# Kernel optimization log

Hardware: AMD Instinct MI355X
Metric: run time of the kernel (lower is better)

Reference implementation:

```python
import jax, jax.numpy as jnp
import numpy as np

N_NODES = 50000
N_EDGES = 300000
D = 256
N_RELS = 500


def setup_inputs() -> dict:
    key = jax.random.key(0)
    ks = jax.random.split(key, 12)
    s = 1.0 / np.sqrt(D)  # keep activations O(1) through the dense transforms
    return {
        "h": jax.random.normal(ks[0], (N_NODES, D), dtype=jnp.float32),
        "prev_h": jax.random.normal(ks[1], (N_NODES, D), dtype=jnp.float32),
        "emb_rel": jax.random.normal(ks[2], (N_RELS, D), dtype=jnp.float32),
        "norm": jax.random.uniform(ks[3], (N_NODES, 1), dtype=jnp.float32),
        "weight_neighbor": jax.random.normal(ks[4], (D, D), dtype=jnp.float32) * s,
        "loop_weight": jax.random.normal(ks[5], (D, D), dtype=jnp.float32) * s,
        "evolve_loop_weight": jax.random.normal(ks[6], (D, D), dtype=jnp.float32) * s,
        "skip_connect_weight": jax.random.normal(ks[7], (D, D), dtype=jnp.float32) * s,
        "skip_connect_bias": jnp.zeros((D,), dtype=jnp.float32),
        "src": jax.random.randint(ks[8], (N_EDGES,), 0, N_NODES),
        "dst": jax.random.randint(ks[9], (N_EDGES,), 0, N_NODES),
        "etype": jax.random.randint(ks[10], (N_EDGES,), 0, N_RELS),
    }


def reference(h, prev_h, emb_rel, norm, weight_neighbor, loop_weight,
              evolve_loop_weight, skip_connect_weight, skip_connect_bias,
              src, dst, etype):
    n_nodes = h.shape[0]
    # msg_func: per-edge gather of src features + relation embedding, dense transform
    msg = (h[src] + emb_rel[etype]) @ weight_neighbor          # [E, D]
    # fn.sum: segment-sum messages into destination nodes
    agg = jax.ops.segment_sum(msg, dst, num_segments=n_nodes)  # [N, D]
    # apply_func: multiply by per-node norm
    agg = agg * norm
    # self-loop: loop_weight where in_degree > 0, evolve_loop_weight otherwise
    in_deg = jax.ops.segment_sum(jnp.ones_like(dst), dst, num_segments=n_nodes)
    has_in = (in_deg > 0)[:, None]
    loop_message = jnp.where(has_in, h @ loop_weight, h @ evolve_loop_weight)
    # skip connection gate
    skip_weight = jax.nn.sigmoid(prev_h @ skip_connect_weight + skip_connect_bias)
    node_repr = skip_weight * (agg + loop_message) + (1.0 - skip_weight) * prev_h
    return jax.nn.relu(node_repr)
```

## Files before the change

### kernel.cpp

```cpp
#include <hip/hip_runtime.h>
#include <hip/hip_bf16.h>
#include <cstdint>
#include <cstddef>

#define N_NODES 50000
#define N_EDGES 300000
#define DIM     256
#define KTOT    768

#define SCAN_BLK  256
#define SCAN_NBLK ((N_NODES + SCAN_BLK - 1) / SCAN_BLK)

typedef unsigned short u16;
typedef __attribute__((ext_vector_type(8))) short short8v;
typedef __attribute__((ext_vector_type(4))) float float4v;

static __device__ __forceinline__ u16 f2bf(float f) {
    union { float f; unsigned u; } v; v.f = f;
    unsigned u = v.u;
    unsigned r = u + 0x7FFFu + ((u >> 16) & 1u);
    return (u16)(r >> 16);
}

__global__ void conv_kernel(const float* __restrict__ h, const float* __restrict__ ph,
                            u16* __restrict__ Xh, u16* __restrict__ Xp) {
    int i = blockIdx.x * blockDim.x + threadIdx.x;
    int e0 = i * 8;
    if (e0 >= 2 * N_NODES * DIM) return;
    const float* src; u16* dst; int off;
    if (e0 < N_NODES * DIM) { src = h;  dst = Xh; off = e0; }
    else                    { src = ph; dst = Xp; off = e0 - N_NODES * DIM; }
    float4 a = *(const float4*)(src + off);
    float4 b = *(const float4*)(src + off + 4);
    u16 o[8] = { f2bf(a.x), f2bf(a.y), f2bf(a.z), f2bf(a.w),
                 f2bf(b.x), f2bf(b.y), f2bf(b.z), f2bf(b.w) };
    *(uint4*)(dst + off) = *(const uint4*)o;
}

__global__ void wt_kernel(const float* __restrict__ Wn, const float* __restrict__ Wl,
                          const float* __restrict__ Wsc, u16* __restrict__ Wt) {
    int k = blockIdx.x;
    int d = threadIdx.x;
    const float* W = (k < 256) ? Wn : ((k < 512) ? Wl : Wsc);
    int kk = k & 255;
    Wt[(size_t)d * KTOT + k] = f2bf(W[kk * DIM + d]);
}

__global__ void hist_kernel(const int* __restrict__ dstv, int* __restrict__ deg) {
    int e = blockIdx.x * 256 + threadIdx.x;
    if (e < N_EDGES) atomicAdd(&deg[dstv[e]], 1);
}

__global__ void scanA_kernel(const int* __restrict__ deg, int* __restrict__ excl_local,
                             int* __restrict__ block_sum) {
    __shared__ int sdata[SCAN_BLK];
    int t = threadIdx.x, i = blockIdx.x * SCAN_BLK + t;
    int v = (i < N_NODES) ? deg[i] : 0;
    sdata[t] = v;
    __syncthreads();
    for (int off = 1; off < SCAN_BLK; off <<= 1) {
        int u = (t >= off) ? sdata[t - off] : 0;
        __syncthreads();
        sdata[t] += u;
        __syncthreads();
    }
    if (i < N_NODES) excl_local[i] = sdata[t] - v;
    if (t == SCAN_BLK - 1) block_sum[blockIdx.x] = sdata[t];
}

__global__ void scanB_kernel(const int* __restrict__ block_sum, int* __restrict__ block_base,
                             int* __restrict__ offsets) {
    __shared__ int sdata[SCAN_NBLK];
    int t = threadIdx.x;
    int v = (t < SCAN_NBLK) ? block_sum[t] : 0;
    if (t < SCAN_NBLK) sdata[t] = v;
    __syncthreads();
    for (int off = 1; off < SCAN_NBLK; off <<= 1) {
        int u = (t >= off && t < SCAN_NBLK) ? sdata[t - off] : 0;
        __syncthreads();
        if (t < SCAN_NBLK) sdata[t] += u;
        __syncthreads();
    }
    if (t < SCAN_NBLK) block_base[t] = sdata[t] - v;
    if (t == SCAN_NBLK - 1) offsets[N_NODES] = sdata[t];
}

__global__ void scanC_kernel(const int* __restrict__ excl_local, const int* __restrict__ block_base,
                             int* __restrict__ offsets, int* __restrict__ cursor) {
    int i = blockIdx.x * SCAN_BLK + threadIdx.x;
    if (i < N_NODES) {
        int e = block_base[blockIdx.x] + excl_local[i];
        offsets[i] = e; cursor[i] = e;
    }
}

__global__ void scatter_kernel(const int* __restrict__ src, const int* __restrict__ dstv,
                               const int* __restrict__ et, int* __restrict__ cursor,
                               int* __restrict__ es, int* __restrict__ ee) {
    int e = blockIdx.x * 256 + threadIdx.x;
    if (e >= N_EDGES) return;
    int d = dstv[e];
    int pos = atomicAdd(&cursor[d], 1);
    es[pos] = src[e];
    ee[pos] = et[e];
}

__global__ void agg_kernel(const float* __restrict__ h, const float* __restrict__ emb,
                           const float* __restrict__ norm, const int* __restrict__ offsets,
                           const int* __restrict__ es, const int* __restrict__ ee,
                           u16* __restrict__ Xa, int* __restrict__ wl_count, int* __restrict__ wl) {
    int wave = (blockIdx.x * 256 + threadIdx.x) >> 6;
    int lane = threadIdx.x & 63;
    if (wave >= N_NODES) return;
    int n = wave;
    int s0 = offsets[n], s1 = offsets[n + 1];
    int c4 = lane * 4;
    float4 acc = make_float4(0.f, 0.f, 0.f, 0.f);
    for (int e = s0; e < s1; e++) {
        int s = es[e], t = ee[e];
        float4 hv = *(const float4*)(h   + (size_t)s * DIM + c4);
        float4 ev = *(const float4*)(emb + (size_t)t * DIM + c4);
        acc.x += hv.x + ev.x; acc.y += hv.y + ev.y;
        acc.z += hv.z + ev.z; acc.w += hv.w + ev.w;
    }
    float nr = norm[n];
    u16 o[4] = { f2bf(acc.x * nr), f2bf(acc.y * nr), f2bf(acc.z * nr), f2bf(acc.w * nr) };
    *(ushort4*)(Xa + (size_t)n * DIM + c4) = *(const ushort4*)o;
    if (lane == 0 && s1 == s0) { int idx = atomicAdd(wl_count, 1); wl[idx] = n; }
}

#define LDSP 72
__launch_bounds__(256, 2)
__global__ void gemm_kernel(const u16* __restrict__ Xa, const u16* __restrict__ Xh,
                            const u16* __restrict__ Xp, const u16* __restrict__ Wt,
                            const float* __restrict__ prev_h, const float* __restrict__ bias,
                            float* __restrict__ out) {
    __shared__ u16 Xs[64 * LDSP];
    __shared__ u16 Ws[256 * LDSP];
    int tid = threadIdx.x;
    int wave = tid >> 6, lane = tid & 63, q = lane >> 4, m16 = lane & 15;
    int m0 = blockIdx.x * 64;

    float4v acc1[4][4], acc2[4][4];
#pragma unroll
    for (int i = 0; i < 4; i++)
#pragma unroll
        for (int j = 0; j < 4; j++) { acc1[i][j] = (float4v)0.f; acc2[i][j] = (float4v)0.f; }

    int xr = tid >> 3, xc = (tid & 7) * 8;
    int wp = tid & 7, wd = tid >> 3;
    int xrow0 = min(m0 + xr, N_NODES - 1);
    int xrow1 = min(m0 + xr + 32, N_NODES - 1);

    for (int kt = 0; kt < 12; kt++) {
        const u16* Xsrc = (kt < 4) ? Xa : ((kt < 8) ? Xh : Xp);
        int koff = (kt & 3) * 64;
        *(uint4*)(&Xs[xr * LDSP + xc]) =
            *(const uint4*)(Xsrc + (size_t)xrow0 * DIM + koff + xc);
        *(uint4*)(&Xs[(xr + 32) * LDSP + xc]) =
            *(const uint4*)(Xsrc + (size_t)xrow1 * DIM + koff + xc);
#pragma unroll
        for (int it = 0; it < 8; it++) {
            int d = wd + it * 32;
            *(uint4*)(&Ws[d * LDSP + wp * 8]) =
                *(const uint4*)(Wt + (size_t)d * KTOT + kt * 64 + wp * 8);
        }
        __syncthreads();
#pragma unroll
        for (int kk = 0; kk < 2; kk++) {
            short8v af[4], bfr[4];
#pragma unroll
            for (int mi = 0; mi < 4; mi++)
                af[mi] = *(const short8v*)(&Xs[(mi * 16 + m16) * LDSP + kk * 32 + q * 8]);
#pragma unroll
            for (int ni = 0; ni < 4; ni++)
                bfr[ni] = *(const short8v*)(&Ws[(wave * 64 + ni * 16 + m16) * LDSP + kk * 32 + q * 8]);
            if (kt < 8) {
#pragma unroll
                for (int mi = 0; mi < 4; mi++)
#pragma unroll
                    for (int ni = 0; ni < 4; ni++)
                        acc1[mi][ni] = __builtin_amdgcn_mfma_f32_16x16x32_bf16(
                            af[mi], bfr[ni], acc1[mi][ni], 0, 0, 0);
            } else {
#pragma unroll
                for (int mi = 0; mi < 4; mi++)
#pragma unroll
                    for (int ni = 0; ni < 4; ni++)
                        acc2[mi][ni] = __builtin_amdgcn_mfma_f32_16x16x32_bf16(
                            af[mi], bfr[ni], acc2[mi][ni], 0, 0, 0);
            }
        }
        __syncthreads();
    }

#pragma unroll
    for (int mi = 0; mi < 4; mi++) {
#pragma unroll
        for (int ni = 0; ni < 4; ni++) {
            int d = wave * 64 + ni * 16 + m16;
            float b = bias[d];
#pragma unroll
            for (int r = 0; r < 4; r++) {
                int node = m0 + mi * 16 + q * 4 + r;
                if (node < N_NODES) {
                    float S  = acc2[mi][ni][r] + b;
                    float sw = 1.f / (1.f + __expf(-S));
                    float ph = prev_h[(size_t)node * DIM + d];
                    float v  = sw * acc1[mi][ni][r] + (1.f - sw) * ph;
                    out[(size_t)node * DIM + d] = fmaxf(v, 0.f);
                }
            }
        }
    }
}

__global__ void fixup_kernel(const float* __restrict__ h, const float* __restrict__ prev_h,
                             const float* __restrict__ We, const float* __restrict__ Wsc,
                             const float* __restrict__ bias, const int* __restrict__ wl_count,
                             const int* __restrict__ wl, float* __restrict__ out) {
    __shared__ float ph[DIM], hh[DIM];
    int d = threadIdx.x;
    int cnt = *wl_count;
    for (int i = blockIdx.x; i < cnt; i += gridDim.x) {
        int n = wl[i];
        ph[d] = prev_h[(size_t)n * DIM + d];
        hh[d] = h[(size_t)n * DIM + d];
        __syncthreads();
        float s = 0.f, l = 0.f;
        for (int k = 0; k < DIM; k++) {
            s += ph[k] * Wsc[k * DIM + d];
            l += hh[k] * We[k * DIM + d];
        }
        float sw = 1.f / (1.f + __expf(-(s + bias[d])));
        float v = sw * l + (1.f - sw) * ph[d];
        out[(size_t)n * DIM + d] = fmaxf(v, 0.f);
        __syncthreads();
    }
}

extern "C" void kernel_launch(void* const* d_in, const int* in_sizes, int n_in,
                              void* d_out, int out_size, void* d_ws, size_t ws_size,
                              hipStream_t stream) {
    const float* h      = (const float*)d_in[0];
    const float* prev_h = (const float*)d_in[1];
    const float* emb    = (const float*)d_in[2];
    const float* norm   = (const float*)d_in[3];
    const float* Wn     = (const float*)d_in[4];
    const float* Wl     = (const float*)d_in[5];
    const float* We     = (const float*)d_in[6];
    const float* Wsc    = (const float*)d_in[7];
    const float* bias   = (const float*)d_in[8];
    const int*   src    = (const int*)d_in[9];
    const int*   dstv   = (const int*)d_in[10];
    const int*   et     = (const int*)d_in[11];
    float* out = (float*)d_out;

    char* ws = (char*)d_ws;
    size_t off = 0;
    auto alloc = [&](size_t bytes) -> char* {
        char* p = ws + off; off += (bytes + 255) & ~(size_t)255; return p;
    };
    u16* Xa      = (u16*)alloc((size_t)N_NODES * DIM * 2);
    u16* Xh      = (u16*)alloc((size_t)N_NODES * DIM * 2);
    u16* Xp      = (u16*)alloc((size_t)N_NODES * DIM * 2);
    u16* Wt      = (u16*)alloc((size_t)DIM * KTOT * 2);
    int* deg     = (int*)alloc((size_t)N_NODES * 4);
    int* wlcnt   = (int*)alloc(16);
    int* wl      = (int*)alloc((size_t)N_NODES * 4);
    int* offsets = (int*)alloc((size_t)(N_NODES + 1) * 4);
    int* cursor  = (int*)alloc((size_t)N_NODES * 4);
    int* es      = (int*)alloc((size_t)N_EDGES * 4);
    int* ee      = (int*)alloc((size_t)N_EDGES * 4);
    int* excl    = (int*)alloc((size_t)N_NODES * 4);
    int* bsum    = (int*)alloc((size_t)SCAN_NBLK * 4);
    int* bbase   = (int*)alloc((size_t)SCAN_NBLK * 4);

    hipMemsetAsync(deg, 0, (size_t)N_NODES * 4, stream);
    hipMemsetAsync(wlcnt, 0, 4, stream);

    conv_kernel<<<(2 * N_NODES * DIM / 8 + 255) / 256, 256, 0, stream>>>(h, prev_h, Xh, Xp);
    wt_kernel<<<KTOT, 256, 0, stream>>>(Wn, Wl, Wsc, Wt);
    hist_kernel<<<(N_EDGES + 255) / 256, 256, 0, stream>>>(dstv, deg);
    scanA_kernel<<<SCAN_NBLK, SCAN_BLK, 0, stream>>>(deg, excl, bsum);
    scanB_kernel<<<1, SCAN_BLK, 0, stream>>>(bsum, bbase, offsets);
    scanC_kernel<<<SCAN_NBLK, SCAN_BLK, 0, stream>>>(excl, bbase, offsets, cursor);
    scatter_kernel<<<(N_EDGES + 255) / 256, 256, 0, stream>>>(src, dstv, et, cursor, es, ee);
    agg_kernel<<<(N_NODES + 3) / 4, 256, 0, stream>>>(h, emb, norm, offsets, es, ee, Xa, wlcnt, wl);
    gemm_kernel<<<(N_NODES + 63) / 64, 256, 0, stream>>>(Xa, Xh, Xp, Wt, prev_h, bias, out);
    fixup_kernel<<<256, 256, 0, stream>>>(h, prev_h, We, Wsc, bias, wlcnt, wl, out);
}
```

Measured before the change: 353.2 us.

## Fuse fp32-to-bf16 conversion into GEMM, pack edge indices, enlarge GEMM tile

Removes the separate conversion kernel by converting h and prev_h rows to bf16 while loading them into shared memory inside the GEMM, which avoids writing and rereading two bf16 copies of the node features. Source index and relation type are packed into one 32-bit word per edge, cutting index traffic in scatter and aggregation at the cost of an integer divide per edge. The GEMM tile grows to 128 rows with 512 threads, so each weight tile is reused across more rows. The fp32 loads into the GEMM are wider than the bf16 loads they replace, and the larger tile leaves fewer blocks.

Measured after the change: 367.9 us. 4.2% more time.

```diff
diff --git a/kernel.cpp b/kernel.cpp
--- a/kernel.cpp
+++ b/kernel.cpp
@@ -7,6 +7,7 @@
 #define N_EDGES 300000
 #define DIM     256
 #define KTOT    768
+#define N_RELS  500
 
 #define SCAN_BLK  256
 #define SCAN_NBLK ((N_NODES + SCAN_BLK - 1) / SCAN_BLK)
@@ -20,21 +21,6 @@
     unsigned u = v.u;
     unsigned r = u + 0x7FFFu + ((u >> 16) & 1u);
     return (u16)(r >> 16);
-}
-
-__global__ void conv_kernel(const float* __restrict__ h, const float* __restrict__ ph,
-                            u16* __restrict__ Xh, u16* __restrict__ Xp) {
-    int i = blockIdx.x * blockDim.x + threadIdx.x;
-    int e0 = i * 8;
-    if (e0 >= 2 * N_NODES * DIM) return;
-    const float* src; u16* dst; int off;
-    if (e0 < N_NODES * DIM) { src = h;  dst = Xh; off = e0; }
-    else                    { src = ph; dst = Xp; off = e0 - N_NODES * DIM; }
-    float4 a = *(const float4*)(src + off);
-    float4 b = *(const float4*)(src + off + 4);
-    u16 o[8] = { f2bf(a.x), f2bf(a.y), f2bf(a.z), f2bf(a.w),
-                 f2bf(b.x), f2bf(b.y), f2bf(b.z), f2bf(b.w) };
-    *(uint4*)(dst + off) = *(const uint4*)o;
 }
 
 __global__ void wt_kernel(const float* __restrict__ Wn, const float* __restrict__ Wl,
@@ -96,18 +82,17 @@
 
 __global__ void scatter_kernel(const int* __restrict__ src, const int* __restrict__ dstv,
                                const int* __restrict__ et, int* __restrict__ cursor,
-                               int* __restrict__ es, int* __restrict__ ee) {
+                               unsigned* __restrict__ esee) {
     int e = blockIdx.x * 256 + threadIdx.x;
     if (e >= N_EDGES) return;
     int d = dstv[e];
     int pos = atomicAdd(&cursor[d], 1);
-    es[pos] = src[e];
-    ee[pos] = et[e];
+    esee[pos] = (unsigned)src[e] * N_RELS + (unsigned)et[e];
 }
 
 __global__ void agg_kernel(const float* __restrict__ h, const float* __restrict__ emb,
                            const float* __restrict__ norm, const int* __restrict__ offsets,
-                           const int* __restrict__ es, const int* __restrict__ ee,
+                           const unsigned* __restrict__ esee,
                            u16* __restrict__ Xa, int* __restrict__ wl_count, int* __restrict__ wl) {
     int wave = (blockIdx.x * 256 + threadIdx.x) >> 6;
     int lane = threadIdx.x & 63;
@@ -117,7 +102,9 @@
     int c4 = lane * 4;
     float4 acc = make_float4(0.f, 0.f, 0.f, 0.f);
     for (int e = s0; e < s1; e++) {
-        int s = es[e], t = ee[e];
+        unsigned v = esee[e];
+        unsigned s = v / N_RELS;
+        unsigned t = v - s * N_RELS;
         float4 hv = *(const float4*)(h   + (size_t)s * DIM + c4);
         float4 ev = *(const float4*)(emb + (size_t)t * DIM + c4);
         acc.x += hv.x + ev.x; acc.y += hv.y + ev.y;
@@ -130,16 +117,17 @@
 }
 
 #define LDSP 72
-__launch_bounds__(256, 2)
-__global__ void gemm_kernel(const u16* __restrict__ Xa, const u16* __restrict__ Xh,
-                            const u16* __restrict__ Xp, const u16* __restrict__ Wt,
-                            const float* __restrict__ prev_h, const float* __restrict__ bias,
-                            float* __restrict__ out) {
-    __shared__ u16 Xs[64 * LDSP];
+__launch_bounds__(512, 4)
+__global__ void gemm_kernel(const u16* __restrict__ Xa, const u16* __restrict__ Wt,
+                            const float* __restrict__ h, const float* __restrict__ prev_h,
+                            const float* __restrict__ bias, float* __restrict__ out) {
+    __shared__ u16 Xs[128 * LDSP];
     __shared__ u16 Ws[256 * LDSP];
     int tid = threadIdx.x;
     int wave = tid >> 6, lane = tid & 63, q = lane >> 4, m16 = lane & 15;
-    int m0 = blockIdx.x * 64;
+    int wm = (wave >> 2) * 64;
+    int wn = (wave & 3) * 64;
+    int m0 = blockIdx.x * 128;
 
     float4v acc1[4][4], acc2[4][4];
 #pragma unroll
@@ -147,23 +135,36 @@
 #pragma unroll
         for (int j = 0; j < 4; j++) { acc1[i][j] = (float4v)0.f; acc2[i][j] = (float4v)0.f; }
 
-    int xr = tid >> 3, xc = (tid & 7) * 8;
-    int wp = tid & 7, wd = tid >> 3;
-    int xrow0 = min(m0 + xr, N_NODES - 1);
-    int xrow1 = min(m0 + xr + 32, N_NODES - 1);
+    int bxr = tid >> 3, bxc = (tid & 7) * 8;
+    int fxr = tid >> 4, fxc = (tid & 15) * 4;
+    int wd  = tid >> 3, wp  = (tid & 7) * 8;
 
     for (int kt = 0; kt < 12; kt++) {
-        const u16* Xsrc = (kt < 4) ? Xa : ((kt < 8) ? Xh : Xp);
         int koff = (kt & 3) * 64;
-        *(uint4*)(&Xs[xr * LDSP + xc]) =
-            *(const uint4*)(Xsrc + (size_t)xrow0 * DIM + koff + xc);
-        *(uint4*)(&Xs[(xr + 32) * LDSP + xc]) =
-            *(const uint4*)(Xsrc + (size_t)xrow1 * DIM + koff + xc);
-#pragma unroll
-        for (int it = 0; it < 8; it++) {
-            int d = wd + it * 32;
-            *(uint4*)(&Ws[d * LDSP + wp * 8]) =
-                *(const uint4*)(Wt + (size_t)d * KTOT + kt * 64 + wp * 8);
+        if (kt < 4) {
+#pragma unroll
+            for (int r = 0; r < 2; r++) {
+                int row = bxr + r * 64;
+                int grow = min(m0 + row, N_NODES - 1);
+                *(uint4*)(&Xs[row * LDSP + bxc]) =
+                    *(const uint4*)(Xa + (size_t)grow * DIM + koff + bxc);
+            }
+        } else {
+            const float* F = (kt < 8) ? h : prev_h;
+#pragma unroll
+            for (int r = 0; r < 4; r++) {
+                int row = fxr + r * 32;
+                int grow = min(m0 + row, N_NODES - 1);
+                float4 fv = *(const float4*)(F + (size_t)grow * DIM + koff + fxc);
+                u16 o[4] = { f2bf(fv.x), f2bf(fv.y), f2bf(fv.z), f2bf(fv.w) };
+                *(ushort4*)(&Xs[row * LDSP + fxc]) = *(const ushort4*)o;
+            }
+        }
+#pragma unroll
+        for (int it = 0; it < 4; it++) {
+            int d = wd + it * 64;
+            *(uint4*)(&Ws[d * LDSP + wp]) =
+                *(const uint4*)(Wt + (size_t)d * KTOT + kt * 64 + wp);
         }
         __syncthreads();
 #pragma unroll
@@ -171,10 +172,10 @@
             short8v af[4], bfr[4];
 #pragma unroll
             for (int mi = 0; mi < 4; mi++)
-                af[mi] = *(const short8v*)(&Xs[(mi * 16 + m16) * LDSP + kk * 32 + q * 8]);
+                af[mi] = *(const short8v*)(&Xs[(wm + mi * 16 + m16) * LDSP + kk * 32 + q * 8]);
 #pragma unroll
             for (int ni = 0; ni < 4; ni++)
-                bfr[ni] = *(const short8v*)(&Ws[(wave * 64 + ni * 16 + m16) * LDSP + kk * 32 + q * 8]);
+                bfr[ni] = *(const short8v*)(&Ws[(wn + ni * 16 + m16) * LDSP + kk * 32 + q * 8]);
             if (kt < 8) {
 #pragma unroll
                 for (int mi = 0; mi < 4; mi++)
@@ -198,11 +199,11 @@
     for (int mi = 0; mi < 4; mi++) {
 #pragma unroll
         for (int ni = 0; ni < 4; ni++) {
-            int d = wave * 64 + ni * 16 + m16;
+            int d = wn + ni * 16 + m16;
             float b = bias[d];
 #pragma unroll
             for (int r = 0; r < 4; r++) {
-                int node = m0 + mi * 16 + q * 4 + r;
+                int node = m0 + wm + mi * 16 + q * 4 + r;
                 if (node < N_NODES) {
                     float S  = acc2[mi][ni][r] + b;
                     float sw = 1.f / (1.f + __expf(-S));
@@ -262,16 +263,13 @@
         char* p = ws + off; off += (bytes + 255) & ~(size_t)255; return p;
     };
     u16* Xa      = (u16*)alloc((size_t)N_NODES * DIM * 2);
-    u16* Xh      = (u16*)alloc((size_t)N_NODES * DIM * 2);
-    u16* Xp      = (u16*)alloc((size_t)N_NODES * DIM * 2);
     u16* Wt      = (u16*)alloc((size_t)DIM * KTOT * 2);
     int* deg     = (int*)alloc((size_t)N_NODES * 4);
     int* wlcnt   = (int*)alloc(16);
     int* wl      = (int*)alloc((size_t)N_NODES * 4);
     int* offsets = (int*)alloc((size_t)(N_NODES + 1) * 4);
     int* cursor  = (int*)alloc((size_t)N_NODES * 4);
-    int* es      = (int*)alloc((size_t)N_EDGES * 4);
-    int* ee      = (int*)alloc((size_t)N_EDGES * 4);
+    unsigned* esee = (unsigned*)alloc((size_t)N_EDGES * 4);
     int* excl    = (int*)alloc((size_t)N_NODES * 4);
     int* bsum    = (int*)alloc((size_t)SCAN_NBLK * 4);
     int* bbase   = (int*)alloc((size_t)SCAN_NBLK * 4);
@@ -279,14 +277,13 @@
     hipMemsetAsync(deg, 0, (size_t)N_NODES * 4, stream);
     hipMemsetAsync(wlcnt, 0, 4, stream);
 
-    conv_kernel<<<(2 * N_NODES * DIM / 8 + 255) / 256, 256, 0, stream>>>(h, prev_h, Xh, Xp);
     wt_kernel<<<KTOT, 256, 0, stream>>>(Wn, Wl, Wsc, Wt);
     hist_kernel<<<(N_EDGES + 255) / 256, 256, 0, stream>>>(dstv, deg);
     scanA_kernel<<<SCAN_NBLK, SCAN_BLK, 0, stream>>>(deg, excl, bsum);
     scanB_kernel<<<1, SCAN_BLK, 0, stream>>>(bsum, bbase, offsets);
     scanC_kernel<<<SCAN_NBLK, SCAN_BLK, 0, stream>>>(excl, bbase, offsets, cursor);
-    scatter_kernel<<<(N_EDGES + 255) / 256, 256, 0, stream>>>(src, dstv, et, cursor, es, ee);
-    agg_kernel<<<(N_NODES + 3) / 4, 256, 0, stream>>>(h, emb, norm, offsets, es, ee, Xa, wlcnt, wl);
-    gemm_kernel<<<(N_NODES + 63) / 64, 256, 0, stream>>>(Xa, Xh, Xp, Wt, prev_h, bias, out);
+    scatter_kernel<<<(N_EDGES + 255) / 256, 256, 0, stream>>>(src, dstv, et, cursor, esee);
+    agg_kernel<<<(N_NODES + 3) / 4, 256, 0, stream>>>(h, emb, norm, offsets, esee, Xa, wlcnt, wl);
+    gemm_kernel<<<(N_NODES + 127) / 128, 512, 0, stream>>>(Xa, Wt, h, prev_h, bias, out);
     fixup_kernel<<<256, 256, 0, stream>>>(h, prev_h, We, Wsc, bias, wlcnt, wl, out);
 }
```

## Gather bf16 features in aggregation, convert prev_h inside GEMM, pack edge indices

Applied to the files above, without the earlier changes.

The aggregation kernel now gathers bf16 copies of h and the relation embeddings, which halves the bytes read per edge. Source and relation indices are packed into one 32-bit word per edge, and the kernel recovers them with a divide by a constant. The separate bf16 conversion pass and buffer for prev_h are removed, and the GEMM converts prev_h from fp32 to bf16 as it stages tiles into LDS. This cuts a full write and re-read of a node-sized buffer, but the GEMM K-loop now reads fp32 from global and spends ALU time converting, and summing bf16-rounded inputs adds a little precision loss.

Result: no change. 346.8 us (-1.8%).

```diff
diff --git a/kernel.cpp b/kernel.cpp
--- a/kernel.cpp
+++ b/kernel.cpp
@@ -7,6 +7,7 @@
 #define N_EDGES 300000
 #define DIM     256
 #define KTOT    768
+#define N_RELS  500
 
 #define SCAN_BLK  256
 #define SCAN_NBLK ((N_NODES + SCAN_BLK - 1) / SCAN_BLK)
@@ -21,15 +22,18 @@
     unsigned r = u + 0x7FFFu + ((u >> 16) & 1u);
     return (u16)(r >> 16);
 }
-
-__global__ void conv_kernel(const float* __restrict__ h, const float* __restrict__ ph,
-                            u16* __restrict__ Xh, u16* __restrict__ Xp) {
+static __device__ __forceinline__ float bf2f(u16 b) {
+    union { unsigned u; float f; } v; v.u = ((unsigned)b) << 16; return v.f;
+}
+
+__global__ void conv_kernel(const float* __restrict__ h, const float* __restrict__ emb,
+                            u16* __restrict__ Xh, u16* __restrict__ embb) {
     int i = blockIdx.x * blockDim.x + threadIdx.x;
     int e0 = i * 8;
-    if (e0 >= 2 * N_NODES * DIM) return;
+    if (e0 >= (N_NODES + N_RELS) * DIM) return;
     const float* src; u16* dst; int off;
-    if (e0 < N_NODES * DIM) { src = h;  dst = Xh; off = e0; }
-    else                    { src = ph; dst = Xp; off = e0 - N_NODES * DIM; }
+    if (e0 < N_NODES * DIM) { src = h;   dst = Xh;   off = e0; }
+    else                    { src = emb; dst = embb; off = e0 - N_NODES * DIM; }
     float4 a = *(const float4*)(src + off);
     float4 b = *(const float4*)(src + off + 4);
     u16 o[8] = { f2bf(a.x), f2bf(a.y), f2bf(a.z), f2bf(a.w),
@@ -96,18 +100,17 @@
 
 __global__ void scatter_kernel(const int* __restrict__ src, const int* __restrict__ dstv,
                                const int* __restrict__ et, int* __restrict__ cursor,
-                               int* __restrict__ es, int* __restrict__ ee) {
+                               unsigned* __restrict__ esee) {
     int e = blockIdx.x * 256 + threadIdx.x;
     if (e >= N_EDGES) return;
     int d = dstv[e];
     int pos = atomicAdd(&cursor[d], 1);
-    es[pos] = src[e];
-    ee[pos] = et[e];
-}
-
-__global__ void agg_kernel(const float* __restrict__ h, const float* __restrict__ emb,
+    esee[pos] = (unsigned)src[e] * N_RELS + (unsigned)et[e];
+}
+
+__global__ void agg_kernel(const u16* __restrict__ Xh, const u16* __restrict__ embb,
                            const float* __restrict__ norm, const int* __restrict__ offsets,
-                           const int* __restrict__ es, const int* __restrict__ ee,
+                           const unsigned* __restrict__ esee,
                            u16* __restrict__ Xa, int* __restrict__ wl_count, int* __restrict__ wl) {
     int wave = (blockIdx.x * 256 + threadIdx.x) >> 6;
     int lane = threadIdx.x & 63;
@@ -117,11 +120,15 @@
     int c4 = lane * 4;
     float4 acc = make_float4(0.f, 0.f, 0.f, 0.f);
     for (int e = s0; e < s1; e++) {
-        int s = es[e], t = ee[e];
-        float4 hv = *(const float4*)(h   + (size_t)s * DIM + c4);
-        float4 ev = *(const float4*)(emb + (size_t)t * DIM + c4);
-        acc.x += hv.x + ev.x; acc.y += hv.y + ev.y;
-        acc.z += hv.z + ev.z; acc.w += hv.w + ev.w;
+        unsigned v = esee[e];
+        unsigned s = v / N_RELS;
+        unsigned t = v - s * N_RELS;
+        ushort4 hv = *(const ushort4*)(Xh   + (size_t)s * DIM + c4);
+        ushort4 ev = *(const ushort4*)(embb + (size_t)t * DIM + c4);
+        acc.x += bf2f(hv.x) + bf2f(ev.x);
+        acc.y += bf2f(hv.y) + bf2f(ev.y);
+        acc.z += bf2f(hv.z) + bf2f(ev.z);
+        acc.w += bf2f(hv.w) + bf2f(ev.w);
     }
     float nr = norm[n];
     u16 o[4] = { f2bf(acc.x * nr), f2bf(acc.y * nr), f2bf(acc.z * nr), f2bf(acc.w * nr) };
@@ -132,13 +139,13 @@
 #define LDSP 72
 __launch_bounds__(256, 2)
 __global__ void gemm_kernel(const u16* __restrict__ Xa, const u16* __restrict__ Xh,
-                            const u16* __restrict__ Xp, const u16* __restrict__ Wt,
-                            const float* __restrict__ prev_h, const float* __restrict__ bias,
-                            float* __restrict__ out) {
+                            const u16* __restrict__ Wt, const float* __restrict__ prev_h,
+                            const float* __restrict__ bias, float* __restrict__ out) {
     __shared__ u16 Xs[64 * LDSP];
     __shared__ u16 Ws[256 * LDSP];
     int tid = threadIdx.x;
     int wave = tid >> 6, lane = tid & 63, q = lane >> 4, m16 = lane & 15;
+    int wn = wave * 64;
     int m0 = blockIdx.x * 64;
 
     float4v acc1[4][4], acc2[4][4];
@@ -148,17 +155,30 @@
         for (int j = 0; j < 4; j++) { acc1[i][j] = (float4v)0.f; acc2[i][j] = (float4v)0.f; }
 
     int xr = tid >> 3, xc = (tid & 7) * 8;
-    int wp = tid & 7, wd = tid >> 3;
+    int wp = tid & 7,  wd = tid >> 3;
     int xrow0 = min(m0 + xr, N_NODES - 1);
     int xrow1 = min(m0 + xr + 32, N_NODES - 1);
 
     for (int kt = 0; kt < 12; kt++) {
-        const u16* Xsrc = (kt < 4) ? Xa : ((kt < 8) ? Xh : Xp);
         int koff = (kt & 3) * 64;
-        *(uint4*)(&Xs[xr * LDSP + xc]) =
-            *(const uint4*)(Xsrc + (size_t)xrow0 * DIM + koff + xc);
-        *(uint4*)(&Xs[(xr + 32) * LDSP + xc]) =
-            *(const uint4*)(Xsrc + (size_t)xrow1 * DIM + koff + xc);
+        if (kt < 8) {
+            const u16* Xsrc = (kt < 4) ? Xa : Xh;
+            *(uint4*)(&Xs[xr * LDSP + xc]) =
+                *(const uint4*)(Xsrc + (size_t)xrow0 * DIM + koff + xc);
+            *(uint4*)(&Xs[(xr + 32) * LDSP + xc]) =
+                *(const uint4*)(Xsrc + (size_t)xrow1 * DIM + koff + xc);
+        } else {
+            const float* p0 = prev_h + (size_t)xrow0 * DIM + koff + xc;
+            const float* p1 = prev_h + (size_t)xrow1 * DIM + koff + xc;
+            float4 a0 = *(const float4*)p0, b0 = *(const float4*)(p0 + 4);
+            float4 a1 = *(const float4*)p1, b1 = *(const float4*)(p1 + 4);
+            u16 o0[8] = { f2bf(a0.x), f2bf(a0.y), f2bf(a0.z), f2bf(a0.w),
+                          f2bf(b0.x), f2bf(b0.y), f2bf(b0.z), f2bf(b0.w) };
+            u16 o1[8] = { f2bf(a1.x), f2bf(a1.y), f2bf(a1.z), f2bf(a1.w),
+                          f2bf(b1.x), f2bf(b1.y), f2bf(b1.z), f2bf(b1.w) };
+            *(uint4*)(&Xs[xr * LDSP + xc])        = *(const uint4*)o0;
+            *(uint4*)(&Xs[(xr + 32) * LDSP + xc]) = *(const uint4*)o1;
+        }
 #pragma unroll
         for (int it = 0; it < 8; it++) {
             int d = wd + it * 32;
@@ -174,7 +194,7 @@
                 af[mi] = *(const short8v*)(&Xs[(mi * 16 + m16) * LDSP + kk * 32 + q * 8]);
 #pragma unroll
             for (int ni = 0; ni < 4; ni++)
-                bfr[ni] = *(const short8v*)(&Ws[(wave * 64 + ni * 16 + m16) * LDSP + kk * 32 + q * 8]);
+                bfr[ni] = *(const short8v*)(&Ws[(wn + ni * 16 + m16) * LDSP + kk * 32 + q * 8]);
             if (kt < 8) {
 #pragma unroll
                 for (int mi = 0; mi < 4; mi++)
@@ -198,7 +218,7 @@
     for (int mi = 0; mi < 4; mi++) {
 #pragma unroll
         for (int ni = 0; ni < 4; ni++) {
-            int d = wave * 64 + ni * 16 + m16;
+            int d = wn + ni * 16 + m16;
             float b = bias[d];
 #pragma unroll
             for (int r = 0; r < 4; r++) {
@@ -263,15 +283,14 @@
     };
     u16* Xa      = (u16*)alloc((size_t)N_NODES * DIM * 2);
     u16* Xh      = (u16*)alloc((size_t)N_NODES * DIM * 2);
-    u16* Xp      = (u16*)alloc((size_t)N_NODES * DIM * 2);
+    u16* embb    = (u16*)alloc((size_t)N_RELS * DIM * 2);
     u16* Wt      = (u16*)alloc((size_t)DIM * KTOT * 2);
     int* deg     = (int*)alloc((size_t)N_NODES * 4);
     int* wlcnt   = (int*)alloc(16);
     int* wl      = (int*)alloc((size_t)N_NODES * 4);
     int* offsets = (int*)alloc((size_t)(N_NODES + 1) * 4);
     int* cursor  = (int*)alloc((size_t)N_NODES * 4);
-    int* es      = (int*)alloc((size_t)N_EDGES * 4);
-    int* ee      = (int*)alloc((size_t)N_EDGES * 4);
+    unsigned* esee = (unsigned*)alloc((size_t)N_EDGES * 4);
     int* excl    = (int*)alloc((size_t)N_NODES * 4);
     int* bsum    = (int*)alloc((size_t)SCAN_NBLK * 4);
     int* bbase   = (int*)alloc((size_t)SCAN_NBLK * 4);
@@ -279,14 +298,14 @@
     hipMemsetAsync(deg, 0, (size_t)N_NODES * 4, stream);
     hipMemsetAsync(wlcnt, 0, 4, stream);
 
-    conv_kernel<<<(2 * N_NODES * DIM / 8 + 255) / 256, 256, 0, stream>>>(h, prev_h, Xh, Xp);
+    conv_kernel<<<((N_NODES + N_RELS) * DIM / 8 + 255) / 256, 256, 0, stream>>>(h, emb, Xh, embb);
     wt_kernel<<<KTOT, 256, 0, stream>>>(Wn, Wl, Wsc, Wt);
     hist_kernel<<<(N_EDGES + 255) / 256, 256, 0, stream>>>(dstv, deg);
     scanA_kernel<<<SCAN_NBLK, SCAN_BLK, 0, stream>>>(deg, excl, bsum);
     scanB_kernel<<<1, SCAN_BLK, 0, stream>>>(bsum, bbase, offsets);
     scanC_kernel<<<SCAN_NBLK, SCAN_BLK, 0, stream>>>(excl, bbase, offsets, cursor);
-    scatter_kernel<<<(N_EDGES + 255) / 256, 256, 0, stream>>>(src, dstv, et, cursor, es, ee);
-    agg_kernel<<<(N_NODES + 3) / 4, 256, 0, stream>>>(h, emb, norm, offsets, es, ee, Xa, wlcnt, wl);
-    gemm_kernel<<<(N_NODES + 63) / 64, 256, 0, stream>>>(Xa, Xh, Xp, Wt, prev_h, bias, out);
+    scatter_kernel<<<(N_EDGES + 255) / 256, 256, 0, stream>>>(src, dstv, et, cursor, esee);
+    agg_kernel<<<(N_NODES + 3) / 4, 256, 0, stream>>>(Xh, embb, norm, offsets, esee, Xa, wlcnt, wl);
+    gemm_kernel<<<(N_NODES + 63) / 64, 256, 0, stream>>>(Xa, Xh, Wt, prev_h, bias, out);
     fixup_kernel<<<256, 256, 0, stream>>>(h, prev_h, We, Wsc, bias, wlcnt, wl, out);
 }
```
